# Optimization experiments

Measured on AMD Instinct MI355X. Metric: run time of the kernel, lower is better.

The kernel has to match this reference:

```python
import jax, jax.numpy as jnp
import numpy as np

EPS = 1e-3
PAD_REC = 7  # filt_size 15 // 2


def conv3d(x, w, pad):
    return jax.lax.conv_general_dilated(
        x, w, (1, 1, 1), [(pad, pad)] * 3,
        dimension_numbers=('NCDHW', 'OIDHW', 'NCDHW'))


def conv2d(x, w, pad):
    return jax.lax.conv_general_dilated(
        x, w, (1, 1), [(pad, pad)] * 2,
        dimension_numbers=('NCHW', 'OIHW', 'NCHW'))


def bn2d(x, g, b):
    # BatchNorm2d with track_running_stats=False: always batch stats, biased var
    m = x.mean(axis=(0, 2, 3), keepdims=True)
    v = x.var(axis=(0, 2, 3), keepdims=True)
    return (x - m) * jax.lax.rsqrt(v + EPS) * g[None, :, None, None] + b[None, :, None, None]


def _ch(p):  # (25,) -> broadcast over NCHW
    return p[None, :, None, None]


def setup_inputs() -> dict:
    key = jax.random.key(0)
    ks = jax.random.split(key, 24)
    C = 25
    d = {}
    d['x'] = jax.random.normal(ks[0], (2, 3, 8, 128, 128), jnp.float32)
    d['conv00_w'] = jax.random.normal(ks[1], (25, 3, 7, 7, 7), jnp.float32) * 0.05
    # conv0 weight overwritten by gabor bank of shape (1, 25, 7, 7, 7): maps 25 -> 1 channel
    d['conv0_w'] = jax.random.normal(ks[2], (1, 25, 7, 7, 7), jnp.float32) * 0.05
    d['conv1_w'] = jax.random.normal(ks[3], (25, 1, 7, 7, 7), jnp.float32) * 0.05
    d['conv1_b'] = jnp.zeros((25,), jnp.float32)
    d['u1_w'] = jax.random.normal(ks[4], (C, C, 1, 1), jnp.float32) * 0.1
    u1_b = jax.random.uniform(ks[5], (C,), jnp.float32, 1.0, 7.0)  # .log() in source is not in-place
    d['u1_b'] = u1_b
    d['u2_w'] = jax.random.normal(ks[6], (C, C, 1, 1), jnp.float32) * 0.1
    d['u2_b'] = -u1_b
    d['w_inh'] = jax.random.normal(ks[7], (C, C, 15, 15), jnp.float32) * 0.02
    d['w_exc'] = jax.random.normal(ks[8], (C, C, 15, 15), jnp.float32) * 0.02
    d['alpha'] = jnp.full((C,), 0.1, jnp.float32)
    d['mu'] = jnp.full((C,), 1.0, jnp.float32)
    d['gamma_p'] = jnp.full((C,), 1.0, jnp.float32)
    d['kappa'] = jnp.full((C,), 0.5, jnp.float32)
    d['w_mix'] = jnp.full((C,), 0.5, jnp.float32)
    d['bn1_w'] = jnp.full((C,), 0.1, jnp.float32)
    d['bn1_b'] = jnp.zeros((C,), jnp.float32)
    d['bn3_w'] = jnp.full((C,), 0.1, jnp.float32)
    d['bn3_b'] = jnp.zeros((C,), jnp.float32)
    d['bn_out_w'] = jnp.ones((C,), jnp.float32)
    d['bn_out_b'] = jnp.zeros((C,), jnp.float32)
    d['fc4_w'] = jax.random.normal(ks[9], (2, 2 * 25 * 64 * 64), jnp.float32) * 0.002
    d['fc4_b'] = jnp.zeros((2,), jnp.float32)
    return d


def reference(x, conv00_w, conv0_w, conv1_w, conv1_b, u1_w, u1_b, u2_w, u2_b,
              w_inh, w_exc, alpha, mu, gamma_p, kappa, w_mix,
              bn1_w, bn1_b, bn3_w, bn3_b, bn_out_w, bn_out_b, fc4_w, fc4_b):
    sp = jax.nn.softplus
    # 3D conv front-end: [2,3,8,128,128] -> [2,25,8,128,128] -> [2,1,...] -> [2,25,...]
    out = conv3d(x, conv00_w, 3)
    out = conv3d(out, conv0_w, 3)
    out = conv3d(out, conv1_w, 3) + conv1_b[None, :, None, None, None]
    out = jnp.square(out)
    out_t = out.transpose(2, 0, 1, 3, 4)  # [T=8, B=2, C=25, 128, 128]

    def step(h, y):
        g1 = jax.nn.sigmoid(conv2d(h, u1_w, 0) + _ch(u1_b))
        c1 = bn2d(conv2d(h * g1, w_inh, PAD_REC), bn1_w, bn1_b)
        ns1 = sp(y - sp(c1 * (_ch(alpha) * h + _ch(mu))))
        g2 = jax.nn.sigmoid(conv2d(ns1, u2_w, 0) + _ch(u2_b))
        c2 = bn2d(conv2d(ns1, w_exc, PAD_REC), bn3_w, bn3_b)
        h2 = sp(_ch(kappa) * ns1 + _ch(gamma_p) * c2 + _ch(w_mix) * ns1 * c2)
        h_new = sp((1.0 - g2) * h + g2 * h2)
        return h_new, None

    h0 = jnp.zeros_like(out_t[0])
    h, _ = jax.lax.scan(step, h0, out_t)

    o = bn2d(h, bn_out_w, bn_out_b)  # [2,25,128,128]
    B, C, H, W = o.shape
    o = o.reshape(B, C, H // 2, 2, W // 2, 2).mean(axis=(3, 5))  # AvgPool2d(2)
    o = o.reshape(1, -1)  # [1, 204800]
    logits = jnp.squeeze(o @ fc4_w.T + fc4_b)  # [2]
    return jax.nn.sigmoid(logits)
```

## Files before the change

### kernel.cpp

```cpp
#include <hip/hip_runtime.h>
#include <cstddef>

#define HW 16384
#define NELEM 819200

#define XT_ROW 4608
#define XT_KS  2304
#define XT_HALF 1152

typedef _Float16 f16x8 __attribute__((ext_vector_type(8)));
typedef _Float16 f16x4 __attribute__((ext_vector_type(4)));
typedef _Float16 f16x2 __attribute__((ext_vector_type(2)));
typedef float    f32x16 __attribute__((ext_vector_type(16)));

#define MFMA32(a, b, c) __builtin_amdgcn_mfma_f32_32x32x16_f16((a), (b), (c), 0, 0, 0)

#if __has_builtin(__builtin_amdgcn_fdot2)
#define HAS_FDOT2 1
#else
#define HAS_FDOT2 0
#endif

__device__ __forceinline__ float sp_f(float x) {
    return fmaxf(x, 0.f) + log1pf(expf(-fabsf(x)));
}
__device__ __forceinline__ float sig_f(float x) {
    return 1.f / (1.f + expf(-x));
}

__global__ __launch_bounds__(256) void xpack0_kernel(
    const float* __restrict__ x, _Float16* __restrict__ x0)
{
    const int p = blockIdx.x * 256 + threadIdx.x;
    const int b = p >> 17, rem = p & 131071;
    const int z = rem >> 14, pix = rem & 16383;
    const int y = pix >> 7, xx = pix & 127;
    const size_t sb = ((size_t)b * 3 * 8 + z) << 14;
    f16x4 v;
    v[0] = (_Float16)x[sb + pix];
    v[1] = (_Float16)x[sb + (8ull << 14) + pix];
    v[2] = (_Float16)x[sb + (16ull << 14) + pix];
    v[3] = (_Float16)0.f;
    *(f16x4*)(x0 + (((size_t)(b * 8 + z) * 134 + y + 3) * 136 + xx + 3) * 4) = v;
}

__global__ __launch_bounds__(256) void repack_w00_kernel(
    const float* __restrict__ w, _Float16* __restrict__ wt)
{
    const int idx = blockIdx.x * 256 + threadIdx.x;
    const int j  = idx & 7;
    const int m  = (idx >> 3) & 31;
    const int h  = (idx >> 8) & 1;
    const int kk = (idx >> 9) & 1;
    const int tapb = idx >> 10;
    const int dz = tapb / 7, dy = tapb - dz * 7;
    const int ic = j & 3, dxl = j >> 2;
    const int dx = kk * 4 + h * 2 + dxl;
    float v = 0.f;
    if (m < 25 && ic < 3 && dx < 7)
        v = w[(((m * 3 + ic) * 7 + dz) * 7 + dy) * 7 + dx];
    wt[idx] = (_Float16)v;
}

__global__ __launch_bounds__(256) void xpack1_kernel(
    const _Float16* __restrict__ b0p, _Float16* __restrict__ x1)
{
    const int p = blockIdx.x * 256 + threadIdx.x;
    const int b = p >> 17, rem = p & 131071;
    const int z = rem >> 14, pix = rem & 16383;
    const int y = pix >> 7, xx = pix & 127;
    float s = 0.f;
    #pragma unroll
    for (int g = 0; g < 25; ++g) s += (float)b0p[(size_t)g * 262144 + p];
    x1[(((size_t)(b * 8 + z) * 134 + y + 3) * 136 + xx + 3) * 2] = (_Float16)s;
}

__global__ __launch_bounds__(256) void repack_w1_kernel(
    const float* __restrict__ w, _Float16* __restrict__ wt)
{
    const int idx = blockIdx.x * 256 + threadIdx.x;
    const int j = idx & 7;
    const int m = (idx >> 3) & 31;
    const int h = (idx >> 8) & 1;
    const int tapb = idx >> 9;
    const int dz = tapb / 7, dy = tapb - dz * 7;
    const int c2 = j & 1, dx = h * 4 + (j >> 1);
    float v = 0.f;
    if (m < 25 && c2 == 0 && dx < 7)
        v = w[((m * 7 + dz) * 7 + dy) * 7 + dx];
    wt[idx] = (_Float16)v;
}

__global__ __launch_bounds__(128) void conv3d00_mfma(
    const _Float16* __restrict__ x0, const _Float16* __restrict__ wt0,
    _Float16* __restrict__ apad)
{
    const int g = blockIdx.x;
    const int b = g >> 10;
    const int zo = (g >> 7) & 7;
    const int y = g & 127;
    const int tid = threadIdx.x;
    const int wv = tid >> 6;
    const int lane = tid & 63;
    const int n = lane & 31;
    const int h = lane >> 5;
    const int xc = wv << 6;

    f32x16 acc0, acc1;
    #pragma unroll
    for (int i = 0; i < 16; ++i) { acc0[i] = 0.f; acc1[i] = 0.f; }

    for (int dz = 0; dz < 7; ++dz) {
        const int zin = zo + dz - 3;
        if (zin < 0 || zin >= 8) continue;
        const _Float16* xpl = x0 + (size_t)(b * 8 + zin) * (134 * 136 * 4);
        #pragma unroll
        for (int dy = 0; dy < 7; ++dy) {
            const _Float16* xr = xpl + (size_t)(y + dy) * (136 * 4);
            const _Float16* wb = wt0 + (size_t)((dz * 7 + dy) * 2) * 512 + h * 256 + n * 8;
            f16x8 a0 = *(const f16x8*)(wb);
            f16x8 a1 = *(const f16x8*)(wb + 512);
            const _Float16* bp = xr + (size_t)(xc + n + 2 * h) * 4;
            f16x8 b00 = *(const f16x8*)(bp);
            f16x8 b01 = *(const f16x8*)(bp + 16);
            f16x8 b10 = *(const f16x8*)(bp + 128);
            f16x8 b11 = *(const f16x8*)(bp + 144);
            acc0 = MFMA32(a0, b00, acc0);
            acc1 = MFMA32(a0, b10, acc1);
            acc0 = MFMA32(a1, b01, acc0);
            acc1 = MFMA32(a1, b11, acc1);
        }
    }
    _Float16* ob = apad + (size_t)((b * 25) * 8 + zo) * 18496
                 + (size_t)(y + 4) * 136 + 4 + xc + n;
    #pragma unroll
    for (int r = 0; r < 16; ++r) {
        const int row = (r & 3) + 8 * (r >> 2) + 4 * h;
        if (row < 25) {
            ob[(size_t)row * 147968]      = (_Float16)acc0[r];
            ob[(size_t)row * 147968 + 32] = (_Float16)acc1[r];
        }
    }
}

__global__ __launch_bounds__(128) void conv3d0_direct(
    const _Float16* __restrict__ apad, const float* __restrict__ wgt,
    _Float16* __restrict__ out)
{
    const int y0 = blockIdx.x * 16;
    const int ic = blockIdx.y;
    const int b  = blockIdx.z >> 3;
    const int zo = blockIdx.z & 7;
    const int tid = threadIdx.x, tx = tid & 15, ty = tid >> 4;

    float acc0[8] = {0,0,0,0,0,0,0,0};
    float acc1[8] = {0,0,0,0,0,0,0,0};
    const float* wb0 = wgt + ic * 343;

    for (int dz = 0; dz < 7; ++dz) {
        const int zin = zo + dz - 3;
        if (zin < 0 || zin >= 8) continue;
        const _Float16* pl = apad + (size_t)((b * 25 + ic) * 8 + zin) * 18496
                           + (size_t)(y0 + (ty << 1) + 1) * 136 + (tx << 3);
        const float* wb = wb0 + dz * 49;
#if HAS_FDOT2
        f16x2 wpn[4], wpo[4];
        #pragma unroll
        for (int j = 0; j <= 7; ++j) {
            f16x8 r0 = *(const f16x8*)(pl + (size_t)j * 136);
            f16x8 r1 = *(const f16x8*)(pl + (size_t)j * 136 + 8);
            _Float16 rr[16];
            #pragma unroll
            for (int i = 0; i < 8; ++i) { rr[i] = r0[i]; rr[8 + i] = r1[i]; }
            f16x2 pr[14];
            #pragma unroll
            for (int i = 0; i < 14; ++i) { pr[i][0] = rr[i + 1]; pr[i][1] = rr[i + 2]; }
            if (j <= 6) {
                #pragma unroll
                for (int p = 0; p < 3; ++p) {
                    wpn[p][0] = (_Float16)wb[j * 7 + 2 * p];
                    wpn[p][1] = (_Float16)wb[j * 7 + 2 * p + 1];
                }
                wpn[3][0] = (_Float16)wb[j * 7 + 6];
                wpn[3][1] = (_Float16)0.f;
            }
            #pragma unroll
            for (int k = 0; k < 8; ++k) {
                if (j <= 6) {
                    #pragma unroll
                    for (int p = 0; p < 4; ++p)
                        acc0[k] = __builtin_amdgcn_fdot2(wpn[p], pr[k + 2 * p], acc0[k], false);
                }
                if (j >= 1) {
                    #pragma unroll
                    for (int p = 0; p < 4; ++p)
                        acc1[k] = __builtin_amdgcn_fdot2(wpo[p], pr[k + 2 * p], acc1[k], false);
                }
            }
            #pragma unroll
            for (int p = 0; p < 4; ++p) wpo[p] = wpn[p];
        }
#else
        float wn[7], wo[7];
        #pragma unroll
        for (int j = 0; j <= 7; ++j) {
            f16x8 r0 = *(const f16x8*)(pl + (size_t)j * 136);
            f16x8 r1 = *(const f16x8*)(pl + (size_t)j * 136 + 8);
            float rrf[16];
            #pragma unroll
            for (int i = 0; i < 8; ++i) { rrf[i] = (float)r0[i]; rrf[8 + i] = (float)r1[i]; }
            if (j <= 6) {
                #pragma unroll
                for (int d = 0; d < 7; ++d) wn[d] = wb[j * 7 + d];
            }
            #pragma unroll
            for (int dx = 0; dx < 7; ++dx) {
                if (j <= 6) {
                    float w0 = wn[dx];
                    #pragma unroll
                    for (int k = 0; k < 8; ++k) acc0[k] = fmaf(rrf[dx + k + 1], w0, acc0[k]);
                }
                if (j >= 1) {
                    float w1 = wo[dx];
                    #pragma unroll
                    for (int k = 0; k < 8; ++k) acc1[k] = fmaf(rrf[dx + k + 1], w1, acc1[k]);
                }
            }
            #pragma unroll
            for (int d = 0; d < 7; ++d) wo[d] = wn[d];
        }
#endif
    }
    _Float16* op = out + (size_t)ic * 262144
              + (((size_t)(b * 8 + zo)) << 14) + ((size_t)(y0 + (ty << 1)) << 7) + (tx << 3);
    f16x8 o0, o1;
    #pragma unroll
    for (int k = 0; k < 8; ++k) { o0[k] = (_Float16)acc0[k]; o1[k] = (_Float16)acc1[k]; }
    *(f16x8*)op = o0;
    *(f16x8*)(op + 128) = o1;
}

__global__ __launch_bounds__(128) void conv3d1_mfma(
    const _Float16* __restrict__ x1, const _Float16* __restrict__ wt1,
    const float* __restrict__ bias, float* __restrict__ out)
{
    const int g = blockIdx.x;
    const int b = g >> 10;
    const int zo = (g >> 7) & 7;
    const int y = g & 127;
    const int tid = threadIdx.x;
    const int wv = tid >> 6;
    const int lane = tid & 63;
    const int n = lane & 31;
    const int h = lane >> 5;
    const int xc = wv << 6;

    f32x16 acc0, acc1;
    #pragma unroll
    for (int i = 0; i < 16; ++i) { acc0[i] = 0.f; acc1[i] = 0.f; }

    for (int dz = 0; dz < 7; ++dz) {
        const int zin = zo + dz - 3;
        if (zin < 0 || zin >= 8) continue;
        const _Float16* xpl = x1 + (size_t)(b * 8 + zin) * (134 * 136 * 2);
        #pragma unroll
        for (int dy = 0; dy < 7; ++dy) {
            const _Float16* wb = wt1 + (size_t)(dz * 7 + dy) * 512 + h * 256 + n * 8;
            f16x8 a0 = *(const f16x8*)(wb);
            const _Float16* bp = xpl + ((size_t)(y + dy) * 136 + xc + n) * 2 + h * 8;
            f16x8 b0 = *(const f16x8*)(bp);
            f16x8 b1 = *(const f16x8*)(bp + 64);
            acc0 = MFMA32(a0, b0, acc0);
            acc1 = MFMA32(a0, b1, acc1);
        }
    }
    float* ob = out + ((((size_t)b * 25) * 8 + zo) << 14) + (y << 7) + xc + n;
    #pragma unroll
    for (int r = 0; r < 16; ++r) {
        const int row = (r & 3) + 8 * (r >> 2) + 4 * h;
        if (row < 25) {
            float v0 = acc0[r] + bias[row];
            float v1 = acc1[r] + bias[row];
            ob[(size_t)row * 131072]      = v0 * v0;
            ob[(size_t)row * 131072 + 32] = v1 * v1;
        }
    }
}

__global__ __launch_bounds__(256) void repack_w_kernel(
    const float* __restrict__ w, _Float16* __restrict__ wt)
{
    const int idx = blockIdx.x * 256 + threadIdx.x;
    const int j    = idx & 7;
    const int m    = (idx >> 3) & 31;
    const int half = (idx >> 8) & 1;
    const int ks   = (idx >> 9) & 1;
    const int t    = idx >> 10;
    const int ic   = ks * 16 + half * 8 + j;
    float v = 0.f;
    if (m < 25 && ic < 25) v = w[(m * 25 + ic) * 225 + t];
    wt[idx] = (_Float16)v;
}

template<int NKY>
__device__ __forceinline__ void conv15_core_v5(
    const _Float16* __restrict__ xb, const _Float16* __restrict__ wtk,
    _Float16* lA, int tid, int bRow0, int xg, int n, int half,
    f32x16& accA, f32x16& accB, f32x16& accC, f32x16& accD)
{
    #pragma unroll
    for (int j = 0; j <= NKY; ++j) {
        if (j < NKY) {
            if (j > 0) __syncthreads();
            _Float16* dst = lA + (size_t)(j & 1) * 15360;
            const _Float16* src = wtk + (size_t)j * 15360;
            #pragma unroll
            for (int p = 0; p < 8; ++p) {
                const int g = p * 256 + tid;
                if (g < 1920)
                    *(f16x8*)(dst + (size_t)g * 8) = *(const f16x8*)(src + (size_t)g * 8);
            }
            __syncthreads();
        }
        const _Float16* br = xb + (size_t)(bRow0 + j) * XT_ROW
                           + (size_t)half * XT_HALF + (size_t)(xg + n) * 8;
        const _Float16* lc = lA + (size_t)(j & 1) * 15360 + half * 256 + n * 8;
        const _Float16* lp = lA + (size_t)((j - 1) & 1) * 15360 + half * 256 + n * 8;
        #pragma unroll
        for (int kx = 0; kx < 15; ++kx) {
            const _Float16* p0 = br + kx * 8;
            f16x8 b00 = *(const f16x8*)(p0);
            f16x8 b01 = *(const f16x8*)(p0 + XT_KS);
            f16x8 b10 = *(const f16x8*)(p0 + 256);
            f16x8 b11 = *(const f16x8*)(p0 + XT_KS + 256);
            if (j < NKY) {
                f16x8 a0 = *(const f16x8*)(lc + kx * 1024);
                f16x8 a1 = *(const f16x8*)(lc + kx * 1024 + 512);
                accA = MFMA32(a0, b00, accA); accA = MFMA32(a1, b01, accA);
                accB = MFMA32(a0, b10, accB); accB = MFMA32(a1, b11, accB);
            }
            if (j >= 1) {
                f16x8 q0 = *(const f16x8*)(lp + kx * 1024);
                f16x8 q1 = *(const f16x8*)(lp + kx * 1024 + 512);
                accC = MFMA32(q0, b00, accC); accC = MFMA32(q1, b01, accC);
                accD = MFMA32(q0, b10, accD); accD = MFMA32(q1, b11, accD);
            }
        }
    }
}

__global__ __launch_bounds__(256) void conv2d15_mfma(
    const _Float16* __restrict__ xt, const _Float16* __restrict__ wt,
    _Float16* __restrict__ cph)
{
    const int blk = blockIdx.x;
    const int b   = blk >> 5;
    const int rq  = blk & 31;
    const int kg  = blockIdx.y;

    __shared__ __align__(16) _Float16 lA[30720];

    const int tid  = threadIdx.x;
    const int w    = tid >> 6;
    const int lane = tid & 63;
    const int n    = lane & 31;
    const int half = lane >> 5;
    const int xg   = (w & 1) << 6;
    const int y0w  = rq * 4 + ((w >> 1) << 1);

    f32x16 accA, accB, accC, accD;
    #pragma unroll
    for (int i = 0; i < 16; ++i) { accA[i] = 0.f; accB[i] = 0.f; accC[i] = 0.f; accD[i] = 0.f; }

    const int ky0 = (kg < 3) ? kg * 4 : 12;
    const _Float16* xb = xt + (size_t)(b * 142) * XT_ROW;
    const _Float16* wtk = wt + (size_t)ky0 * 15360;
    const int bRow0 = y0w + ky0;

    if (kg < 3) conv15_core_v5<4>(xb, wtk, lA, tid, bRow0, xg, n, half, accA, accB, accC, accD);
    else        conv15_core_v5<3>(xb, wtk, lA, tid, bRow0, xg, n, half, accA, accB, accC, accD);

    _Float16* ob = cph + (size_t)kg * NELEM + (((size_t)b * 25) << 14) + (y0w << 7) + xg + n;
    #pragma unroll
    for (int r = 0; r < 16; ++r) {
        const int oc = (r & 3) + 8 * (r >> 2) + 4 * half;
        if (oc < 25) {
            _Float16* p = ob + ((size_t)oc << 14);
            p[0]   = (_Float16)accA[r];
            p[32]  = (_Float16)accB[r];
            p[128] = (_Float16)accC[r];
            p[160] = (_Float16)accD[r];
        }
    }
}

__global__ __launch_bounds__(256) void bnstats1_kernel(
    const _Float16* __restrict__ cph, _Float16* __restrict__ csh,
    float2* __restrict__ ps)
{
    const int c = blockIdx.x;
    const int s = blockIdx.y;
    const int tid = threadIdx.x;
    float s1 = 0.f, s2 = 0.f;
    #pragma unroll
    for (int bb = 0; bb < 2; ++bb) {
        const size_t plane = ((size_t)(bb * 25 + c)) << 14;
        #pragma unroll
        for (int i = 0; i < 2; ++i) {
            const size_t e = plane + ((size_t)(s * 512 + tid + i * 256)) * 4;
            float4 v = make_float4(0.f, 0.f, 0.f, 0.f);
            #pragma unroll
            for (int p = 0; p < 4; ++p) {
                f16x4 q = *(const f16x4*)(cph + (size_t)p * NELEM + e);
                v.x += (float)q[0]; v.y += (float)q[1]; v.z += (float)q[2]; v.w += (float)q[3];
            }
            f16x4 o;
            o[0] = (_Float16)v.x; o[1] = (_Float16)v.y; o[2] = (_Float16)v.z; o[3] = (_Float16)v.w;
            *(f16x4*)(csh + e) = o;
            s1 += v.x + v.y + v.z + v.w;
            s2 += v.x * v.x + v.y * v.y + v.z * v.z + v.w * v.w;
        }
    }
    #pragma unroll
    for (int off = 32; off; off >>= 1) { s1 += __shfl_down(s1, off); s2 += __shfl_down(s2, off); }
    __shared__ float a1[4], a2[4];
    if ((tid & 63) == 0) { a1[tid >> 6] = s1; a2[tid >> 6] = s2; }
    __syncthreads();
    if (tid == 0)
        ps[c * 8 + s] = make_float2(a1[0] + a1[1] + a1[2] + a1[3],
                                    a2[0] + a2[1] + a2[2] + a2[3]);
}

__global__ __launch_bounds__(256) void nsg_kernel(
    const float* __restrict__ y, const float* __restrict__ h,
    const _Float16* __restrict__ csh, const float2* __restrict__ ps,
    const float* __restrict__ gw, const float* __restrict__ gb,
    const float* __restrict__ alpha, const float* __restrict__ mu,
    _Float16* __restrict__ xt, int t)
{
    __shared__ float sc[25], sh[25];
    const int tid = threadIdx.x;
    if (tid < 25) {
        float s1 = 0.f, s2 = 0.f;
        #pragma unroll
        for (int s = 0; s < 8; ++s) { float2 v = ps[tid * 8 + s]; s1 += v.x; s2 += v.y; }
        const float m = s1 * (1.f / 32768.f);
        const float var = fmaxf(s2 * (1.f / 32768.f) - m * m, 0.f);
        const float scv = gw[tid] * rsqrtf(var + 1e-3f);
        sc[tid] = scv;
        sh[tid] = gb[tid] - m * scv;
    }
    __syncthreads();
    const int p = blockIdx.x * 256 + tid;
    const int b = p >> 14, pix = p & (HW - 1);
    const size_t base = (((size_t)b * 25) << 14) + pix;
    __align__(16) _Float16 xv[32];
    #pragma unroll
    for (int c = 0; c < 25; ++c) {
        const size_t idx = base + ((size_t)c << 14);
        const float yv = y[(((size_t)(b * 25 + c) * 8 + t) << 14) + pix];
        const float c1n = (float)csh[idx] * sc[c] + sh[c];
        const float pre = c1n * (alpha[c] * h[idx] + mu[c]);
        xv[c] = (_Float16)sp_f(yv - sp_f(pre));
    }
    #pragma unroll
    for (int c = 25; c < 32; ++c) xv[c] = (_Float16)0.f;
    const int yy = pix >> 7, xx = pix & 127;
    _Float16* xp = xt + (size_t)(b * 142 + yy + 7) * XT_ROW + (size_t)(xx + 7) * 8;
    *(float4*)(xp)                   = ((const float4*)xv)[0];
    *(float4*)(xp + XT_HALF)         = ((const float4*)xv)[1];
    *(float4*)(xp + XT_KS)           = ((const float4*)xv)[2];
    *(float4*)(xp + XT_KS + XT_HALF) = ((const float4*)xv)[3];
}

__global__ __launch_bounds__(256) void hg_kernel(
    float* __restrict__ h, const _Float16* __restrict__ csh,
    const float2* __restrict__ ps, const float* __restrict__ gw,
    const float* __restrict__ gb, const float* __restrict__ kappa,
    const float* __restrict__ gp, const float* __restrict__ wmix,
    const float* __restrict__ u1w, const float* __restrict__ u1b,
    const float* __restrict__ u2w, const float* __restrict__ u2b,
    _Float16* __restrict__ xt)
{
    __shared__ float sc[25], sh[25];
    const int tid = threadIdx.x;
    if (tid < 25) {
        float s1 = 0.f, s2 = 0.f;
        #pragma unroll
        for (int s = 0; s < 8; ++s) { float2 v = ps[tid * 8 + s]; s1 += v.x; s2 += v.y; }
        const float m = s1 * (1.f / 32768.f);
        const float var = fmaxf(s2 * (1.f / 32768.f) - m * m, 0.f);
        const float scv = gw[tid] * rsqrtf(var + 1e-3f);
        sc[tid] = scv;
        sh[tid] = gb[tid] - m * scv;
    }
    __syncthreads();
    const int p = blockIdx.x * 256 + tid;
    const int b = p >> 14, pix = p & (HW - 1);
    const size_t base = (((size_t)b * 25) << 14) + pix;
    const int yy = pix >> 7, xx = pix & 127;
    _Float16* xp = xt + (size_t)(b * 142 + yy + 7) * XT_ROW + (size_t)(xx + 7) * 8;
    __align__(16) _Float16 nvh[32];
    ((float4*)nvh)[0] = *(const float4*)(xp);
    ((float4*)nvh)[1] = *(const float4*)(xp + XT_HALF);
    ((float4*)nvh)[2] = *(const float4*)(xp + XT_KS);
    ((float4*)nvh)[3] = *(const float4*)(xp + XT_KS + XT_HALF);
    float nv[25];
    #pragma unroll
    for (int c = 0; c < 25; ++c) nv[c] = (float)nvh[c];
    float g2v[25];
    #pragma unroll
    for (int oc = 0; oc < 25; ++oc) {
        float acc = u2b[oc];
        #pragma unroll
        for (int ic = 0; ic < 25; ++ic) acc += u2w[oc * 25 + ic] * nv[ic];
        g2v[oc] = sig_f(acc);
    }
    float hv[25];
    #pragma unroll
    for (int c = 0; c < 25; ++c) {
        const size_t idx = base + ((size_t)c << 14);
        const float c2n = (float)csh[idx] * sc[c] + sh[c];
        const float n = nv[c];
        const float h2 = sp_f(kappa[c] * n + gp[c] * c2n + wmix[c] * n * c2n);
        const float g = g2v[c];
        const float hn = sp_f((1.f - g) * h[idx] + g * h2);
        hv[c] = hn;
        h[idx] = hn;
    }
    __align__(16) _Float16 xv[32];
    #pragma unroll
    for (int oc = 0; oc < 25; ++oc) {
        float acc = u1b[oc];
        #pragma unroll
        for (int ic = 0; ic < 25; ++ic) acc += u1w[oc * 25 + ic] * hv[ic];
        xv[oc] = (_Float16)(hv[oc] * sig_f(acc));
    }
    #pragma unroll
    for (int oc = 25; oc < 32; ++oc) xv[oc] = (_Float16)0.f;
    *(float4*)(xp)                   = ((const float4*)xv)[0];
    *(float4*)(xp + XT_HALF)         = ((const float4*)xv)[1];
    *(float4*)(xp + XT_KS)           = ((const float4*)xv)[2];
    *(float4*)(xp + XT_KS + XT_HALF) = ((const float4*)xv)[3];
}

__global__ __launch_bounds__(256) void bnstats_head_kernel(
    const float* __restrict__ x, float2* __restrict__ ps)
{
    const int c = blockIdx.x;
    const int s = blockIdx.y;
    const int tid = threadIdx.x;
    float s1 = 0.f, s2 = 0.f;
    #pragma unroll
    for (int bb = 0; bb < 2; ++bb) {
        const size_t plane = ((size_t)(bb * 25 + c)) << 14;
        const float4* p0 = (const float4*)(x + plane) + s * 512;
        #pragma unroll
        for (int i = 0; i < 2; ++i) {
            float4 v = p0[tid + i * 256];
            s1 += v.x + v.y + v.z + v.w;
            s2 += v.x * v.x + v.y * v.y + v.z * v.z + v.w * v.w;
        }
    }
    #pragma unroll
    for (int off = 32; off; off >>= 1) { s1 += __shfl_down(s1, off); s2 += __shfl_down(s2, off); }
    __shared__ float a1[4], a2[4];
    if ((tid & 63) == 0) { a1[tid >> 6] = s1; a2[tid >> 6] = s2; }
    __syncthreads();
    if (tid == 0)
        ps[c * 8 + s] = make_float2(a1[0] + a1[1] + a1[2] + a1[3],
                                    a2[0] + a2[1] + a2[2] + a2[3]);
}

__global__ __launch_bounds__(256) void fc1_kernel(
    const float* __restrict__ h, const float2* __restrict__ ps,
    const float* __restrict__ gw, const float* __restrict__ gb,
    const float* __restrict__ fcw, float2* __restrict__ part)
{
    __shared__ float sc[25], sh[25];
    const int tid = threadIdx.x;
    if (tid < 25) {
        float s1 = 0.f, s2 = 0.f;
        #pragma unroll
        for (int s = 0; s < 8; ++s) { float2 v = ps[tid * 8 + s]; s1 += v.x; s2 += v.y; }
        const float m = s1 * (1.f / 32768.f);
        const float var = fmaxf(s2 * (1.f / 32768.f) - m * m, 0.f);
        const float scv = gw[tid] * rsqrtf(var + 1e-3f);
        sc[tid] = scv;
        sh[tid] = gb[tid] - m * scv;
    }
    __syncthreads();
    const int i = blockIdx.x * 256 + tid;
    int px = i & 63;
    int t = i >> 6;
    int py = t & 63; t >>= 6;
    int c = t >= 25 ? t - 25 : t;
    const float* hp = h + ((size_t)t << 14);
    const int y0 = py << 1, xg = px << 1;
    float s = hp[(y0 << 7) + xg] + hp[(y0 << 7) + xg + 1]
            + hp[((y0 + 1) << 7) + xg] + hp[((y0 + 1) << 7) + xg + 1];
    const float o = 0.25f * s * sc[c] + sh[c];
    float p0 = o * fcw[i];
    float p1 = o * fcw[204800 + i];
    #pragma unroll
    for (int off = 32; off; off >>= 1) { p0 += __shfl_down(p0, off); p1 += __shfl_down(p1, off); }
    __shared__ float a0[4], a1[4];
    if ((tid & 63) == 0) { a0[tid >> 6] = p0; a1[tid >> 6] = p1; }
    __syncthreads();
    if (tid == 0)
        part[blockIdx.x] = make_float2(a0[0] + a0[1] + a0[2] + a0[3],
                                       a1[0] + a1[1] + a1[2] + a1[3]);
}

__global__ __launch_bounds__(256) void fc2_kernel(
    const float2* __restrict__ part, const float* __restrict__ fcb, float* __restrict__ out)
{
    const int tid = threadIdx.x;
    float s0 = 0.f, s1 = 0.f;
    for (int i = tid; i < 800; i += 256) { float2 v = part[i]; s0 += v.x; s1 += v.y; }
    #pragma unroll
    for (int off = 32; off; off >>= 1) { s0 += __shfl_down(s0, off); s1 += __shfl_down(s1, off); }
    __shared__ float a0[4], a1[4];
    if ((tid & 63) == 0) { a0[tid >> 6] = s0; a1[tid >> 6] = s1; }
    __syncthreads();
    if (tid == 0) {
        out[0] = sig_f(a0[0] + a0[1] + a0[2] + a0[3] + fcb[0]);
        out[1] = sig_f(a1[0] + a1[1] + a1[2] + a1[3] + fcb[1]);
    }
}

extern "C" void kernel_launch(void* const* d_in, const int* in_sizes, int n_in,
                              void* d_out, int out_size, void* d_ws, size_t ws_size,
                              hipStream_t stream)
{
    const float* x        = (const float*)d_in[0];
    const float* conv00_w = (const float*)d_in[1];
    const float* conv0_w  = (const float*)d_in[2];
    const float* conv1_w  = (const float*)d_in[3];
    const float* conv1_b  = (const float*)d_in[4];
    const float* u1_w     = (const float*)d_in[5];
    const float* u1_b     = (const float*)d_in[6];
    const float* u2_w     = (const float*)d_in[7];
    const float* u2_b     = (const float*)d_in[8];
    const float* w_inh    = (const float*)d_in[9];
    const float* w_exc    = (const float*)d_in[10];
    const float* alpha    = (const float*)d_in[11];
    const float* mu       = (const float*)d_in[12];
    const float* gamma_p  = (const float*)d_in[13];
    const float* kappa    = (const float*)d_in[14];
    const float* w_mix    = (const float*)d_in[15];
    const float* bn1_w    = (const float*)d_in[16];
    const float* bn1_b    = (const float*)d_in[17];
    const float* bn3_w    = (const float*)d_in[18];
    const float* bn3_b    = (const float*)d_in[19];
    const float* bn_out_w = (const float*)d_in[20];
    const float* bn_out_b = (const float*)d_in[21];
    const float* fc4_w    = (const float*)d_in[22];
    const float* fc4_b    = (const float*)d_in[23];

    float* ws = (float*)d_ws;
    float* Y    = ws;
    float* R    = ws + 6553600;
    float* X0f  = ws + 13107200;
    float* X1f  = ws + 13690624;
    float* WT0f = ws + 13982336;
    float* WT1cf= ws + 14007424;
    float* WT1f = ws + 14019968;
    float* WT2f = ws + 14135168;
    float* XTf  = ws + 14250368;
    float* PART = ws + 14904704;
    float* PS   = PART + 1600;

    _Float16* B0p = (_Float16*)Y;
    float* H    = R;
    _Float16* CPH = (_Float16*)(R + 819200);
    _Float16* CSH = (_Float16*)(R + 2457600);

    _Float16* APAD = (_Float16*)R;
    _Float16* X0  = (_Float16*)X0f;
    _Float16* X1  = (_Float16*)X1f;
    _Float16* WT0 = (_Float16*)WT0f;
    _Float16* WT1c= (_Float16*)WT1cf;
    _Float16* WT1 = (_Float16*)WT1f;
    _Float16* WT2 = (_Float16*)WT2f;
    _Float16* XT  = (_Float16*)XTf;

    (void)hipMemsetAsync(APAD, 0, (size_t)7398400 * sizeof(_Float16), stream);
    (void)hipMemsetAsync(X0, 0, (size_t)1166848 * sizeof(_Float16), stream);
    (void)hipMemsetAsync(X1, 0, (size_t)583424 * sizeof(_Float16), stream);
    (void)hipMemsetAsync(XT, 0, (size_t)1308672 * sizeof(_Float16), stream);
    xpack0_kernel<<<1024, 256, 0, stream>>>(x, X0);
    repack_w00_kernel<<<196, 256, 0, stream>>>(conv00_w, WT0);
    repack_w1_kernel<<<98, 256, 0, stream>>>(conv1_w, WT1c);
    repack_w_kernel<<<900, 256, 0, stream>>>(w_inh, WT1);
    repack_w_kernel<<<900, 256, 0, stream>>>(w_exc, WT2);

    conv3d00_mfma<<<2048, 128, 0, stream>>>(X0, WT0, APAD);
    conv3d0_direct<<<dim3(8, 25, 16), 128, 0, stream>>>(APAD, conv0_w, B0p);
    xpack1_kernel<<<1024, 256, 0, stream>>>(B0p, X1);
    conv3d1_mfma<<<2048, 128, 0, stream>>>(X1, WT1c, conv1_b, Y);

    (void)hipMemsetAsync(H, 0, (size_t)NELEM * sizeof(float), stream);
    for (int t = 0; t < 8; ++t) {
        conv2d15_mfma<<<dim3(64, 4), 256, 0, stream>>>(XT, WT1, CPH);
        bnstats1_kernel<<<dim3(25, 8), 256, 0, stream>>>(CPH, CSH, (float2*)PS);
        nsg_kernel<<<128, 256, 0, stream>>>(Y, H, CSH, (const float2*)PS, bn1_w, bn1_b,
                                            alpha, mu, XT, t);
        conv2d15_mfma<<<dim3(64, 4), 256, 0, stream>>>(XT, WT2, CPH);
        bnstats1_kernel<<<dim3(25, 8), 256, 0, stream>>>(CPH, CSH, (float2*)PS);
        hg_kernel<<<128, 256, 0, stream>>>(H, CSH, (const float2*)PS, bn3_w, bn3_b,
                                           kappa, gamma_p, w_mix, u1_w, u1_b,
                                           u2_w, u2_b, XT);
    }

    bnstats_head_kernel<<<dim3(25, 8), 256, 0, stream>>>(H, (float2*)PS);
    fc1_kernel<<<800, 256, 0, stream>>>(H, (const float2*)PS, bn_out_w, bn_out_b,
                                        fc4_w, (float2*)PART);
    fc2_kernel<<<1, 256, 0, stream>>>((const float2*)PART, fc4_b, (float*)d_out);
}
```

Measured before the change: 1.104 ms.

## Split channels across two threads per pixel in nsg and hg kernels

The nsg and hg elementwise kernels now assign two threads per pixel, each handling half the channels (0-15 and 16-24), and the grid is doubled to 256 blocks. In hg, per-pixel channel vectors are exchanged through shared memory so each thread can compute its slice of the 1x1 gate convolutions, which adds two barriers. The aim is to raise parallelism and cut per-thread register pressure in these small kernels, which previously launched only 128 blocks. The cost is extra shared-memory traffic and synchronisation.

```diff
diff --git a/kernel.cpp b/kernel.cpp
--- a/kernel.cpp
+++ b/kernel.cpp
@@ -451,26 +451,29 @@
         sh[tid] = gb[tid] - m * scv;
     }
     __syncthreads();
-    const int p = blockIdx.x * 256 + tid;
+    const int slot = tid >> 7;
+    const int p = blockIdx.x * 128 + (tid & 127);
     const int b = p >> 14, pix = p & (HW - 1);
     const size_t base = (((size_t)b * 25) << 14) + pix;
-    __align__(16) _Float16 xv[32];
-    #pragma unroll
-    for (int c = 0; c < 25; ++c) {
+    const int c0 = slot ? 16 : 0, c1 = slot ? 25 : 16;
+    __align__(16) _Float16 xv[16];
+    #pragma unroll 16
+    for (int c = c0; c < c1; ++c) {
         const size_t idx = base + ((size_t)c << 14);
         const float yv = y[(((size_t)(b * 25 + c) * 8 + t) << 14) + pix];
         const float c1n = (float)csh[idx] * sc[c] + sh[c];
         const float pre = c1n * (alpha[c] * h[idx] + mu[c]);
-        xv[c] = (_Float16)sp_f(yv - sp_f(pre));
-    }
-    #pragma unroll
-    for (int c = 25; c < 32; ++c) xv[c] = (_Float16)0.f;
+        xv[c - c0] = (_Float16)sp_f(yv - sp_f(pre));
+    }
+    if (slot) {
+        #pragma unroll
+        for (int c = 9; c < 16; ++c) xv[c] = (_Float16)0.f;
+    }
     const int yy = pix >> 7, xx = pix & 127;
-    _Float16* xp = xt + (size_t)(b * 142 + yy + 7) * XT_ROW + (size_t)(xx + 7) * 8;
-    *(float4*)(xp)                   = ((const float4*)xv)[0];
-    *(float4*)(xp + XT_HALF)         = ((const float4*)xv)[1];
-    *(float4*)(xp + XT_KS)           = ((const float4*)xv)[2];
-    *(float4*)(xp + XT_KS + XT_HALF) = ((const float4*)xv)[3];
+    _Float16* xp = xt + (size_t)(b * 142 + yy + 7) * XT_ROW + (size_t)(xx + 7) * 8
+                 + (size_t)slot * XT_KS;
+    *(float4*)(xp)           = ((const float4*)xv)[0];
+    *(float4*)(xp + XT_HALF) = ((const float4*)xv)[1];
 }
 
 __global__ __launch_bounds__(256) void hg_kernel(
@@ -483,6 +486,8 @@
     _Float16* __restrict__ xt)
 {
     __shared__ float sc[25], sh[25];
+    __shared__ float nvs[128 * 26];
+    __shared__ float hvs[128 * 26];
     const int tid = threadIdx.x;
     if (tid < 25) {
         float s1 = 0.f, s2 = 0.f;
@@ -494,54 +499,55 @@
         sc[tid] = scv;
         sh[tid] = gb[tid] - m * scv;
     }
-    __syncthreads();
-    const int p = blockIdx.x * 256 + tid;
+    const int slot = tid >> 7;
+    const int lpix = tid & 127;
+    const int p = blockIdx.x * 128 + lpix;
     const int b = p >> 14, pix = p & (HW - 1);
     const size_t base = (((size_t)b * 25) << 14) + pix;
     const int yy = pix >> 7, xx = pix & 127;
-    _Float16* xp = xt + (size_t)(b * 142 + yy + 7) * XT_ROW + (size_t)(xx + 7) * 8;
-    __align__(16) _Float16 nvh[32];
+    _Float16* xp = xt + (size_t)(b * 142 + yy + 7) * XT_ROW + (size_t)(xx + 7) * 8
+                 + (size_t)slot * XT_KS;
+    const int c0 = slot ? 16 : 0, c1 = slot ? 25 : 16;
+    float* nvr = nvs + lpix * 26;
+    float* hvr = hvs + lpix * 26;
+
+    __align__(16) _Float16 nvh[16];
     ((float4*)nvh)[0] = *(const float4*)(xp);
     ((float4*)nvh)[1] = *(const float4*)(xp + XT_HALF);
-    ((float4*)nvh)[2] = *(const float4*)(xp + XT_KS);
-    ((float4*)nvh)[3] = *(const float4*)(xp + XT_KS + XT_HALF);
-    float nv[25];
-    #pragma unroll
-    for (int c = 0; c < 25; ++c) nv[c] = (float)nvh[c];
-    float g2v[25];
-    #pragma unroll
-    for (int oc = 0; oc < 25; ++oc) {
-        float acc = u2b[oc];
-        #pragma unroll
-        for (int ic = 0; ic < 25; ++ic) acc += u2w[oc * 25 + ic] * nv[ic];
-        g2v[oc] = sig_f(acc);
-    }
-    float hv[25];
-    #pragma unroll
-    for (int c = 0; c < 25; ++c) {
+    #pragma unroll 16
+    for (int c = c0; c < c1; ++c) nvr[c] = (float)nvh[c - c0];
+    __syncthreads();
+
+    #pragma unroll 16
+    for (int c = c0; c < c1; ++c) {
+        float acc = u2b[c];
+        #pragma unroll
+        for (int ic = 0; ic < 25; ++ic) acc += u2w[c * 25 + ic] * nvr[ic];
+        const float g = sig_f(acc);
         const size_t idx = base + ((size_t)c << 14);
         const float c2n = (float)csh[idx] * sc[c] + sh[c];
-        const float n = nv[c];
+        const float n = nvr[c];
         const float h2 = sp_f(kappa[c] * n + gp[c] * c2n + wmix[c] * n * c2n);
-        const float g = g2v[c];
         const float hn = sp_f((1.f - g) * h[idx] + g * h2);
-        hv[c] = hn;
         h[idx] = hn;
-    }
-    __align__(16) _Float16 xv[32];
-    #pragma unroll
-    for (int oc = 0; oc < 25; ++oc) {
-        float acc = u1b[oc];
-        #pragma unroll
-        for (int ic = 0; ic < 25; ++ic) acc += u1w[oc * 25 + ic] * hv[ic];
-        xv[oc] = (_Float16)(hv[oc] * sig_f(acc));
-    }
-    #pragma unroll
-    for (int oc = 25; oc < 32; ++oc) xv[oc] = (_Float16)0.f;
-    *(float4*)(xp)                   = ((const float4*)xv)[0];
-    *(float4*)(xp + XT_HALF)         = ((const float4*)xv)[1];
-    *(float4*)(xp + XT_KS)           = ((const float4*)xv)[2];
-    *(float4*)(xp + XT_KS + XT_HALF) = ((const float4*)xv)[3];
+        hvr[c] = hn;
+    }
+    __syncthreads();
+
+    __align__(16) _Float16 xv[16];
+    #pragma unroll 16
+    for (int c = c0; c < c1; ++c) {
+        float acc = u1b[c];
+        #pragma unroll
+        for (int ic = 0; ic < 25; ++ic) acc += u1w[c * 25 + ic] * hvr[ic];
+        xv[c - c0] = (_Float16)(hvr[c] * sig_f(acc));
+    }
+    if (slot) {
+        #pragma unroll
+        for (int c = 9; c < 16; ++c) xv[c] = (_Float16)0.f;
+    }
+    *(float4*)(xp)           = ((const float4*)xv)[0];
+    *(float4*)(xp + XT_HALF) = ((const float4*)xv)[1];
 }
 
 __global__ __launch_bounds__(256) void bnstats_head_kernel(
@@ -704,11 +710,11 @@
     for (int t = 0; t < 8; ++t) {
         conv2d15_mfma<<<dim3(64, 4), 256, 0, stream>>>(XT, WT1, CPH);
         bnstats1_kernel<<<dim3(25, 8), 256, 0, stream>>>(CPH, CSH, (float2*)PS);
-        nsg_kernel<<<128, 256, 0, stream>>>(Y, H, CSH, (const float2*)PS, bn1_w, bn1_b,
+        nsg_kernel<<<256, 256, 0, stream>>>(Y, H, CSH, (const float2*)PS, bn1_w, bn1_b,
                                             alpha, mu, XT, t);
         conv2d15_mfma<<<dim3(64, 4), 256, 0, stream>>>(XT, WT2, CPH);
         bnstats1_kernel<<<dim3(25, 8), 256, 0, stream>>>(CPH, CSH, (float2*)PS);
-        hg_kernel<<<128, 256, 0, stream>>>(H, CSH, (const float2*)PS, bn3_w, bn3_b,
+        hg_kernel<<<256, 256, 0, stream>>>(H, CSH, (const float2*)PS, bn3_w, bn3_b,
                                            kappa, gamma_p, w_mix, u1_w, u1_b,
                                            u2_w, u2_b, XT);
     }
```

Result: slower. 1.130 ms (+2.3%).
